# Optimization experiments

Hardware: AMD Instinct MI355X
Metric: run time of the kernel (lower is better)

Reference implementation:

```python
import jax, jax.numpy as jnp
import numpy as np

N, E, D, H, C = 20000, 320000, 128, 4, 128
NEG_SLOPE = 0.2

def _ln(x, g, b, eps=1e-5):
    mu = x.mean(-1, keepdims=True)
    var = ((x - mu) ** 2).mean(-1, keepdims=True)
    return (x - mu) * jax.lax.rsqrt(var + eps) * g + b

def _gatv2(x, src, dst, Wl, bl, Wr, br, att, b):
    # PyG GATv2Conv, concat=False (mean over heads), dropout off (eval)
    n = x.shape[0]
    xl = (x @ Wl + bl).reshape(n, H, C)   # source transform
    xr = (x @ Wr + br).reshape(n, H, C)   # destination transform
    e = jax.nn.leaky_relu(xl[src] + xr[dst], NEG_SLOPE)      # [E,H,C]
    score = jnp.einsum('ehc,hc->eh', e, att)                 # [E,H]
    m = jax.ops.segment_max(score, dst, num_segments=n)      # per-dst max
    w = jnp.exp(score - m[dst])
    denom = jax.ops.segment_sum(w, dst, num_segments=n)
    alpha = w / (denom[dst] + 1e-16)                         # softmax over incoming edges
    out = jax.ops.segment_sum(alpha[:, :, None] * xl[src], dst, num_segments=n)  # [N,H,C]
    return out.mean(axis=1) + b

def setup_inputs() -> dict:
    key = jax.random.key(0)
    ks = jax.random.split(key, 34)
    s = 1.0 / np.sqrt(D)
    def w(k, shape):
        return jax.random.normal(k, shape, jnp.float32) * s
    inp = {
        'x': jax.random.normal(ks[0], (N, D), jnp.float32),
        'edge_index': jax.random.randint(ks[1], (2, E), 0, N, jnp.int32),
        'W_in': w(ks[2], (D, C)), 'b_in': jnp.zeros((C,), jnp.float32),
        'c1_Wl': w(ks[3], (C, H * C)), 'c1_bl': jnp.zeros((H * C,), jnp.float32),
        'c1_Wr': w(ks[4], (C, H * C)), 'c1_br': jnp.zeros((H * C,), jnp.float32),
        'c1_att': w(ks[5], (H, C)), 'c1_b': jnp.zeros((C,), jnp.float32),
        'ln1_g': jnp.ones((C,), jnp.float32), 'ln1_b': jnp.zeros((C,), jnp.float32),
        'a_Wl': w(ks[6], (C, H * C)), 'a_bl': jnp.zeros((H * C,), jnp.float32),
        'a_Wr': w(ks[7], (C, H * C)), 'a_br': jnp.zeros((H * C,), jnp.float32),
        'a_att': w(ks[8], (H, C)), 'a_b': jnp.zeros((C,), jnp.float32),
        'aln_g': jnp.ones((C,), jnp.float32), 'aln_b': jnp.zeros((C,), jnp.float32),
        'ah_W': w(ks[9], (C, 1)), 'ah_b': jnp.zeros((1,), jnp.float32),
        'k_Wl': w(ks[10], (C, H * C)), 'k_bl': jnp.zeros((H * C,), jnp.float32),
        'k_Wr': w(ks[11], (C, H * C)), 'k_br': jnp.zeros((H * C,), jnp.float32),
        'k_att': w(ks[12], (H, C)), 'k_b': jnp.zeros((C,), jnp.float32),
        'kln_g': jnp.ones((C,), jnp.float32), 'kln_b': jnp.zeros((C,), jnp.float32),
        'kh_W': w(ks[13], (C, 1)), 'kh_b': jnp.zeros((1,), jnp.float32),
    }
    return inp

def reference(x, edge_index, W_in, b_in,
              c1_Wl, c1_bl, c1_Wr, c1_br, c1_att, c1_b, ln1_g, ln1_b,
              a_Wl, a_bl, a_Wr, a_br, a_att, a_b, aln_g, aln_b, ah_W, ah_b,
              k_Wl, k_bl, k_Wr, k_br, k_att, k_b, kln_g, kln_b, kh_W, kh_b):
    n = x.shape[0]
    loops = jnp.arange(n, dtype=edge_index.dtype)
    src = jnp.concatenate([edge_index[0], loops])  # PyG adds self-loops by default
    dst = jnp.concatenate([edge_index[1], loops])
    h = jax.nn.relu(x @ W_in + b_in)
    h_res = _gatv2(h, src, dst, c1_Wl, c1_bl, c1_Wr, c1_br, c1_att, c1_b)
    h = jax.nn.relu(_ln(h + h_res, ln1_g, ln1_b))
    xa = _gatv2(h, src, dst, a_Wl, a_bl, a_Wr, a_br, a_att, a_b)
    xa = jax.nn.relu(_ln(xa + h, aln_g, aln_b))
    action_logits = (xa @ ah_W + ah_b).squeeze(-1)
    xc = _gatv2(h, src, dst, k_Wl, k_bl, k_Wr, k_br, k_att, k_b)
    xc = jax.nn.relu(_ln(xc + h, kln_g, kln_b))
    state_value = xc @ kh_W + kh_b
    return action_logits, state_value
```

## Files before the change

### kernel.cpp

```cpp
#include <hip/hip_runtime.h>
#include <hip/hip_bf16.h>

typedef __hip_bfloat16 bf16;
typedef __attribute__((ext_vector_type(8))) short short8;
typedef __attribute__((ext_vector_type(4))) short short4_t;
typedef __attribute__((ext_vector_type(4))) float float4_t;
typedef __attribute__((ext_vector_type(2))) float float2v;
typedef __attribute__((ext_vector_type(2))) unsigned int uint2v;

__device__ __forceinline__ short f2bs(float f) {
    bf16 b = __float2bfloat16(f);
    return *(short*)&b;
}

template <int CTRL>
__device__ __forceinline__ float dpp_addf(float x) {
    int s = __builtin_amdgcn_update_dpp(
        0, __builtin_bit_cast(int, x), CTRL, 0xf, 0xf, true);
    return x + __builtin_bit_cast(float, s);
}
__device__ __forceinline__ float rowsum16(float x) {
    x = dpp_addf<0xB1>(x);
    x = dpp_addf<0x4E>(x);
    x = dpp_addf<0x141>(x);
    x = dpp_addf<0x140>(x);
    return x;
}

__global__ __launch_bounds__(256) void count_kernel(const int* __restrict__ ei,
                                                    int* __restrict__ cnt,
                                                    int E, int N, int NB) {
    int e = blockIdx.x * 256 + threadIdx.x;
    if (e >= E + N) return;
    int s, d;
    if (e < E) { s = ei[e]; d = ei[(size_t)E + e]; }
    else       { s = e - E; d = e - E; }
    atomicAdd(&cnt[(size_t)d * NB + (s >> 10)], 1);
}

__global__ __launch_bounds__(256) void scan_blk_kernel(const int* __restrict__ cnt,
                                                       int* __restrict__ rowptr,
                                                       int* __restrict__ bsum, int M) {
    __shared__ int ts[256];
    const int tid = threadIdx.x;
    const int idx = blockIdx.x * 1024 + tid * 4;
    int v[4];
    int s = 0;
#pragma unroll
    for (int i = 0; i < 4; ++i) {
        int j = idx + i;
        v[i] = (j < M) ? cnt[j] : 0;
        s += v[i];
    }
    ts[tid] = s;
    __syncthreads();
    for (int off = 1; off < 256; off <<= 1) {
        int t = (tid >= off) ? ts[tid - off] : 0;
        __syncthreads();
        ts[tid] += t;
        __syncthreads();
    }
    int run = (tid == 0) ? 0 : ts[tid - 1];
    if (tid == 255) bsum[blockIdx.x] = ts[255];
#pragma unroll
    for (int i = 0; i < 4; ++i) {
        int j = idx + i;
        if (j < M) rowptr[j] = run;
        run += v[i];
    }
}

__global__ __launch_bounds__(1024) void scan_top_kernel(int* __restrict__ bsum, int NBLK) {
    __shared__ int ps[1024];
    const int tid = threadIdx.x;
    int v = (tid < NBLK) ? bsum[tid] : 0;
    ps[tid] = v;
    __syncthreads();
    for (int off = 1; off < 1024; off <<= 1) {
        int t = (tid >= off) ? ps[tid - off] : 0;
        __syncthreads();
        ps[tid] += t;
        __syncthreads();
    }
    int ex = (tid == 0) ? 0 : ps[tid - 1];
    if (tid < NBLK) bsum[tid] = ex;
}

__global__ __launch_bounds__(256) void scan_add_kernel(int* __restrict__ rowptr,
                                                       const int* __restrict__ bsum,
                                                       int M, int ET) {
    int idx = blockIdx.x * 256 + threadIdx.x;
    if (idx < M) rowptr[idx] += bsum[idx >> 10];
    if (idx == 0) rowptr[M] = ET;
}

__global__ __launch_bounds__(256) void scatter_kernel(const int* __restrict__ ei,
                                                      const int* __restrict__ rowptr,
                                                      int* __restrict__ cursor,
                                                      int* __restrict__ csr_off,
                                                      int E, int N, int NB) {
    int e = blockIdx.x * 256 + threadIdx.x;
    if (e >= E + N) return;
    int s, d;
    if (e < E) { s = ei[e]; d = ei[(size_t)E + e]; }
    else       { s = e - E; d = e - E; }
    size_t b = (size_t)d * NB + (s >> 10);
    int pos = atomicAdd(&cursor[b], 1);
    csr_off[rowptr[b] + pos] = s * 4096;
}

__global__ __launch_bounds__(256) void transpose_w_kernel(
        const float* __restrict__ W_in,
        const float* __restrict__ c1_Wl, const float* __restrict__ c1_Wr,
        const float* __restrict__ a_Wl, const float* __restrict__ a_Wr,
        const float* __restrict__ k_Wl, const float* __restrict__ k_Wr,
        bf16* __restrict__ Wt,
        const float* __restrict__ c1_bl, const float* __restrict__ c1_br,
        const float* __restrict__ a_bl, const float* __restrict__ a_br,
        const float* __restrict__ k_bl, const float* __restrict__ k_br,
        float* __restrict__ b1, float* __restrict__ bak) {
    if (blockIdx.z == 7) {
        int flat = blockIdx.y * 16 + blockIdx.x;
        if (flat >= 12) return;
        int i = flat * 256 + threadIdx.x;
        if (i < 1024) {
            b1[i] = (i < 512) ? c1_bl[i] : c1_br[i - 512];
        } else if (i < 3072) {
            int j = i - 1024;
            const float* b = (j < 512) ? a_bl : (j < 1024) ? a_br
                           : (j < 1536) ? k_bl : k_br;
            bak[j] = b[j & 511];
        }
        return;
    }
    __shared__ float tile[32][33];
    const float* src; int nc, drow;
    switch (blockIdx.z) {
        case 0: src = W_in;  nc = 128; drow = 0;    break;
        case 1: src = c1_Wl; nc = 512; drow = 128;  break;
        case 2: src = c1_Wr; nc = 512; drow = 640;  break;
        case 3: src = a_Wl;  nc = 512; drow = 1152; break;
        case 4: src = a_Wr;  nc = 512; drow = 1664; break;
        case 5: src = k_Wl;  nc = 512; drow = 2176; break;
        default: src = k_Wr; nc = 512; drow = 2688; break;
    }
    const int n0 = blockIdx.x * 32;
    if (n0 >= nc) return;
    const int k0 = blockIdx.y * 32;
    const int tx = threadIdx.x & 31, ty = threadIdx.x >> 5;
#pragma unroll
    for (int i = 0; i < 4; ++i)
        tile[ty + i * 8][tx] = src[(size_t)(k0 + ty + i * 8) * nc + n0 + tx];
    __syncthreads();
#pragma unroll
    for (int i = 0; i < 4; ++i)
        Wt[(size_t)(drow + n0 + ty + i * 8) * 128 + k0 + tx] =
            __float2bfloat16(tile[tx][ty + i * 8]);
}

__global__ __launch_bounds__(256, 2) void gemm_mfma_kernel(
        const float* __restrict__ A, const bf16* __restrict__ Ab,
        const bf16* __restrict__ Wt,
        const float* __restrict__ bias,
        float* __restrict__ outF, bf16* __restrict__ outB,
        int M, int ldc, int relu) {
    __shared__ short As[128][136];
    __shared__ short Bs[128][136];
    const int tid = threadIdx.x;
    const int m0 = blockIdx.x * 128;
    const int n0 = blockIdx.y * 128;

    if (Ab) {
        short8 zero8;
#pragma unroll
        for (int q = 0; q < 8; ++q) zero8[q] = 0;
#pragma unroll
        for (int i = 0; i < 8; ++i) {
            int idx = i * 256 + tid;
            int r = idx >> 4, k8 = (idx & 15) * 8;
            int gm = m0 + r;
            short8 s = (gm < M) ? *(const short8*)&Ab[(size_t)gm * 128 + k8] : zero8;
            *(short8*)&As[r][k8] = s;
        }
    } else {
#pragma unroll
        for (int i = 0; i < 16; ++i) {
            int idx = i * 256 + tid;
            int r = idx >> 5, k4 = (idx & 31) * 4;
            int gm = m0 + r;
            float4 v = (gm < M) ? *(const float4*)&A[(size_t)gm * 128 + k4]
                                : make_float4(0.f, 0.f, 0.f, 0.f);
            short4_t s;
            s.x = f2bs(v.x); s.y = f2bs(v.y); s.z = f2bs(v.z); s.w = f2bs(v.w);
            *(short4_t*)&As[r][k4] = s;
        }
    }
#pragma unroll
    for (int i = 0; i < 8; ++i) {
        int idx = i * 256 + tid;
        int nr = idx >> 4, k8 = (idx & 15) * 8;
        *(short8*)&Bs[nr][k8] = *(const short8*)&Wt[(size_t)(n0 + nr) * 128 + k8];
    }
    __syncthreads();

    const int lane = tid & 63;
    const int w = tid >> 6;
    const int wm = (w >> 1) * 64, wn = (w & 1) * 64;
    const int fr = lane & 15;
    const int fq = (lane >> 4) * 8;

    float4_t acc[4][4] = {};
#pragma unroll
    for (int kk = 0; kk < 128; kk += 32) {
        short8 a[4], b[4];
#pragma unroll
        for (int t = 0; t < 4; ++t) a[t] = *(const short8*)&As[wm + t * 16 + fr][kk + fq];
#pragma unroll
        for (int t = 0; t < 4; ++t) b[t] = *(const short8*)&Bs[wn + t * 16 + fr][kk + fq];
#pragma unroll
        for (int ti = 0; ti < 4; ++ti)
#pragma unroll
            for (int tj = 0; tj < 4; ++tj)
                acc[ti][tj] = __builtin_amdgcn_mfma_f32_16x16x32_bf16(
                    a[ti], b[tj], acc[ti][tj], 0, 0, 0);
    }

    const int r0 = (lane >> 4) * 4;
#pragma unroll
    for (int ti = 0; ti < 4; ++ti) {
#pragma unroll
        for (int tj = 0; tj < 4; ++tj) {
            int col = n0 + wn + tj * 16 + fr;
            float bz = bias[col];
#pragma unroll
            for (int r = 0; r < 4; ++r) {
                size_t row = m0 + wm + ti * 16 + r0 + r;
                float v = acc[ti][tj][r] + bz;
                if (relu) v = fmaxf(v, 0.f);
                if (outF) outF[row * ldc + col] = v;
                if (outB) outB[row * ldc + col] = __float2bfloat16(v);
            }
        }
    }
}

__global__ __launch_bounds__(256) void gat_kernel(
        const bf16* __restrict__ xl, const bf16* __restrict__ xr,
        const float* __restrict__ att,
        const int* __restrict__ rowptr, const int* __restrict__ csr_off,
        const float* __restrict__ h_res,
        const float* __restrict__ gbias,
        const float* __restrict__ ln_g, const float* __restrict__ ln_b,
        float* __restrict__ h_out, bf16* __restrict__ h_outb, int N, int NB) {
    const int n = blockIdx.x * 4 + (threadIdx.x >> 6);
    if (n >= N) return;
    const int lane = threadIdx.x & 63;
    const int sl = lane & 15;
    const int hc = (lane >> 4) * 128 + sl * 8;

    float2v a2[4], xr2[4];
    {
        const float* ap = att + hc;
        short8 v = *(const short8*)(xr + (size_t)n * 2048 + hc);
        const unsigned int* uv = (const unsigned int*)&v;
#pragma unroll
        for (int j = 0; j < 4; ++j) {
            a2[j].x = ap[2 * j]; a2[j].y = ap[2 * j + 1];
            unsigned u = uv[j];
            xr2[j].x = __uint_as_float(u << 16);
            xr2[j].y = __uint_as_float(u & 0xffff0000u);
        }
    }
    const int rs = rowptr[(size_t)n * NB];
    const int re = rowptr[(size_t)n * NB + NB];
    const char* xlh = (const char*)xl + (size_t)hc * 2;

    float l = 0.f;
    float2v acc2[4] = {};
    int o0 = csr_off[rs];
    short8 va = *(const short8*)(xlh + o0);
    int o1 = (rs + 1 < re) ? csr_off[rs + 1] : o0;
    short8 vb = *(const short8*)(xlh + o1);
    int o2 = (rs + 2 < re) ? csr_off[rs + 2] : o0;

    for (int e = rs; e < re; ++e) {
        short8 cur = va; va = vb;
        if (e + 2 < re) {
            vb = *(const short8*)(xlh + o2);
            o2 = (e + 3 < re) ? csr_off[e + 3] : o0;
        }
        const unsigned int* uv = (const unsigned int*)&cur;
        float2v pa = {0.f, 0.f}, pb = {0.f, 0.f};
        float2v xs[4];
#pragma unroll
        for (int j = 0; j < 4; ++j) {
            unsigned u = uv[j];
            float2v x;
            x.x = __uint_as_float(u << 16);
            x.y = __uint_as_float(u & 0xffff0000u);
            xs[j] = x;
            float2v t = x + xr2[j];
            float2v ta = __builtin_bit_cast(float2v,
                           __builtin_bit_cast(uint2v, t) & 0x7fffffffu);
            pa = __builtin_elementwise_fma(a2[j], t, pa);
            pb = __builtin_elementwise_fma(a2[j], ta, pb);
        }
        float p = rowsum16(0.6f * (pa.x + pa.y) + 0.4f * (pb.x + pb.y));
        float wv = __expf(fminf(p, 60.f));
        l += wv;
        float2v ws = {wv, wv};
#pragma unroll
        for (int j = 0; j < 4; ++j)
            acc2[j] = __builtin_elementwise_fma(ws, xs[j], acc2[j]);
    }

    float* accf = (float*)acc2;
    const float inv = 0.25f / (l + 1e-16f);
#pragma unroll
    for (int j = 0; j < 8; ++j) accf[j] *= inv;
#pragma unroll
    for (int off = 16; off <= 32; off <<= 1)
#pragma unroll
        for (int j = 0; j < 8; ++j) accf[j] += __shfl_xor(accf[j], off, 64);

    if (lane < 16) {
        const int cb = sl * 8;
        const float* hr = h_res + (size_t)n * 128 + cb;
        float vv[8];
#pragma unroll
        for (int j = 0; j < 8; ++j) vv[j] = accf[j] + gbias[cb + j] + hr[j];
        float t1 = 0.f, t2 = 0.f;
#pragma unroll
        for (int j = 0; j < 8; ++j) { t1 += vv[j]; t2 += vv[j] * vv[j]; }
        const float s1 = rowsum16(t1), s2 = rowsum16(t2);
        const float mu   = s1 * 0.0078125f;
        const float var  = s2 * 0.0078125f - mu * mu;
        const float rstd = rsqrtf(var + 1e-5f);
        float y[8];
#pragma unroll
        for (int j = 0; j < 8; ++j) {
            y[j] = fmaf((vv[j] - mu) * rstd, ln_g[cb + j], ln_b[cb + j]);
            y[j] = fmaxf(y[j], 0.f);
        }
        *(float4*)(h_out + (size_t)n * 128 + cb) = make_float4(y[0], y[1], y[2], y[3]);
        *(float4*)(h_out + (size_t)n * 128 + cb + 4) = make_float4(y[4], y[5], y[6], y[7]);
        short8 yb;
#pragma unroll
        for (int j = 0; j < 8; ++j) yb[j] = f2bs(y[j]);
        *(short8*)(h_outb + (size_t)n * 128 + cb) = yb;
    }
}

__global__ __launch_bounds__(256) void gat2_kernel(
        const bf16* __restrict__ cat,
        const float* __restrict__ a_att, const float* __restrict__ k_att,
        const int* __restrict__ rowptr, const int* __restrict__ csr_off,
        const float* __restrict__ h_res,
        const float* __restrict__ a_gb, const float* __restrict__ k_gb,
        const float* __restrict__ aln_g, const float* __restrict__ aln_b,
        const float* __restrict__ kln_g, const float* __restrict__ kln_b,
        const float* __restrict__ ah_W, const float* __restrict__ ah_b,
        const float* __restrict__ kh_W, const float* __restrict__ kh_b,
        float* __restrict__ out_logits, float* __restrict__ out_value,
        int N, int NB) {
    const int n = blockIdx.x * 4 + (threadIdx.x >> 6);
    if (n >= N) return;
    const int lane = threadIdx.x & 63;
    const int sl = lane & 15;
    const int hc = (lane >> 4) * 128 + sl * 8;

    float2v aa[4], ak[4], xra[4], xrk[4];
    {
        const float* apa = a_att + hc;
        const float* apk = k_att + hc;
        short8 vra = *(const short8*)(cat + (size_t)n * 2048 + 512 + hc);
        short8 vrk = *(const short8*)(cat + (size_t)n * 2048 + 1536 + hc);
        const unsigned int* ua = (const unsigned int*)&vra;
        const unsigned int* uk = (const unsigned int*)&vrk;
#pragma unroll
        for (int j = 0; j < 4; ++j) {
            aa[j].x = apa[2 * j]; aa[j].y = apa[2 * j + 1];
            ak[j].x = apk[2 * j]; ak[j].y = apk[2 * j + 1];
            unsigned u = ua[j];
            xra[j].x = __uint_as_float(u << 16);
            xra[j].y = __uint_as_float(u & 0xffff0000u);
            u = uk[j];
            xrk[j].x = __uint_as_float(u << 16);
            xrk[j].y = __uint_as_float(u & 0xffff0000u);
        }
    }
    const int rs = rowptr[(size_t)n * NB];
    const int re = rowptr[(size_t)n * NB + NB];
    const char* xlh = (const char*)cat + (size_t)hc * 2;

    float la = 0.f, lk = 0.f;
    float2v acca[4] = {}, acck[4] = {};
    int o0 = csr_off[rs];
    short8 vaa = *(const short8*)(xlh + o0);
    short8 vak = *(const short8*)(xlh + o0 + 2048);
    int o1 = (rs + 1 < re) ? csr_off[rs + 1] : o0;
    short8 vba = *(const short8*)(xlh + o1);
    short8 vbk = *(const short8*)(xlh + o1 + 2048);
    int o2 = (rs + 2 < re) ? csr_off[rs + 2] : o0;

    for (int e = rs; e < re; ++e) {
        short8 ca = vaa, ck = vak;
        vaa = vba; vak = vbk;
        if (e + 2 < re) {
            vba = *(const short8*)(xlh + o2);
            vbk = *(const short8*)(xlh + o2 + 2048);
            o2 = (e + 3 < re) ? csr_off[e + 3] : o0;
        }
        const unsigned int* ua = (const unsigned int*)&ca;
        const unsigned int* uk = (const unsigned int*)&ck;
        float2v paa = {0.f, 0.f}, pba = {0.f, 0.f};
        float2v pak = {0.f, 0.f}, pbk = {0.f, 0.f};
        float2v xsa[4], xsk[4];
#pragma unroll
        for (int j = 0; j < 4; ++j) {
            unsigned u = ua[j];
            float2v x;
            x.x = __uint_as_float(u << 16);
            x.y = __uint_as_float(u & 0xffff0000u);
            xsa[j] = x;
            float2v t = x + xra[j];
            float2v ta = __builtin_bit_cast(float2v,
                           __builtin_bit_cast(uint2v, t) & 0x7fffffffu);
            paa = __builtin_elementwise_fma(aa[j], t, paa);
            pba = __builtin_elementwise_fma(aa[j], ta, pba);

            u = uk[j];
            x.x = __uint_as_float(u << 16);
            x.y = __uint_as_float(u & 0xffff0000u);
            xsk[j] = x;
            t = x + xrk[j];
            ta = __builtin_bit_cast(float2v,
                   __builtin_bit_cast(uint2v, t) & 0x7fffffffu);
            pak = __builtin_elementwise_fma(ak[j], t, pak);
            pbk = __builtin_elementwise_fma(ak[j], ta, pbk);
        }
        float p_a = rowsum16(0.6f * (paa.x + paa.y) + 0.4f * (pba.x + pba.y));
        float p_k = rowsum16(0.6f * (pak.x + pak.y) + 0.4f * (pbk.x + pbk.y));
        float wa = __expf(fminf(p_a, 60.f));
        float wk = __expf(fminf(p_k, 60.f));
        la += wa; lk += wk;
        float2v wsa = {wa, wa}, wsk = {wk, wk};
#pragma unroll
        for (int j = 0; j < 4; ++j) {
            acca[j] = __builtin_elementwise_fma(wsa, xsa[j], acca[j]);
            acck[j] = __builtin_elementwise_fma(wsk, xsk[j], acck[j]);
        }
    }

    float* afa = (float*)acca;
    float* afk = (float*)acck;
    const float inva = 0.25f / (la + 1e-16f);
    const float invk = 0.25f / (lk + 1e-16f);
#pragma unroll
    for (int j = 0; j < 8; ++j) { afa[j] *= inva; afk[j] *= invk; }
#pragma unroll
    for (int off = 16; off <= 32; off <<= 1)
#pragma unroll
        for (int j = 0; j < 8; ++j) {
            afa[j] += __shfl_xor(afa[j], off, 64);
            afk[j] += __shfl_xor(afk[j], off, 64);
        }

    if (lane < 32) {
        const int cb = sl * 8;
        const float* hr = h_res + (size_t)n * 128 + cb;
        float hrv[8];
#pragma unroll
        for (int j = 0; j < 8; ++j) hrv[j] = hr[j];
        if (lane < 16) {
            float vv[8];
#pragma unroll
            for (int j = 0; j < 8; ++j) vv[j] = afa[j] + a_gb[cb + j] + hrv[j];
            float t1 = 0.f, t2 = 0.f;
#pragma unroll
            for (int j = 0; j < 8; ++j) { t1 += vv[j]; t2 += vv[j] * vv[j]; }
            const float s1 = rowsum16(t1), s2 = rowsum16(t2);
            const float mu   = s1 * 0.0078125f;
            const float var  = s2 * 0.0078125f - mu * mu;
            const float rstd = rsqrtf(var + 1e-5f);
            float d = 0.f;
#pragma unroll
            for (int j = 0; j < 8; ++j) {
                float y = fmaf((vv[j] - mu) * rstd, aln_g[cb + j], aln_b[cb + j]);
                d += fmaxf(y, 0.f) * ah_W[cb + j];
            }
            d = rowsum16(d);
            if (sl == 0) out_logits[n] = d + ah_b[0];
        } else {
            float vv[8];
#pragma unroll
            for (int j = 0; j < 8; ++j) vv[j] = afk[j] + k_gb[cb + j] + hrv[j];
            float t1 = 0.f, t2 = 0.f;
#pragma unroll
            for (int j = 0; j < 8; ++j) { t1 += vv[j]; t2 += vv[j] * vv[j]; }
            const float s1 = rowsum16(t1), s2 = rowsum16(t2);
            const float mu   = s1 * 0.0078125f;
            const float var  = s2 * 0.0078125f - mu * mu;
            const float rstd = rsqrtf(var + 1e-5f);
            float d = 0.f;
#pragma unroll
            for (int j = 0; j < 8; ++j) {
                float y = fmaf((vv[j] - mu) * rstd, kln_g[cb + j], kln_b[cb + j]);
                d += fmaxf(y, 0.f) * kh_W[cb + j];
            }
            d = rowsum16(d);
            if (sl == 0) out_value[n] = d + kh_b[0];
        }
    }
}

extern "C" void kernel_launch(void* const* d_in, const int* in_sizes, int n_in,
                              void* d_out, int out_size, void* d_ws, size_t ws_size,
                              hipStream_t stream) {
    const float* x      = (const float*)d_in[0];
    const int*   ei     = (const int*)  d_in[1];
    const float* W_in   = (const float*)d_in[2];
    const float* b_in   = (const float*)d_in[3];
    const float* c1_Wl  = (const float*)d_in[4];
    const float* c1_bl  = (const float*)d_in[5];
    const float* c1_Wr  = (const float*)d_in[6];
    const float* c1_br  = (const float*)d_in[7];
    const float* c1_att = (const float*)d_in[8];
    const float* c1_b   = (const float*)d_in[9];
    const float* ln1_g  = (const float*)d_in[10];
    const float* ln1_b  = (const float*)d_in[11];
    const float* a_Wl   = (const float*)d_in[12];
    const float* a_bl   = (const float*)d_in[13];
    const float* a_Wr   = (const float*)d_in[14];
    const float* a_br   = (const float*)d_in[15];
    const float* a_att  = (const float*)d_in[16];
    const float* a_b    = (const float*)d_in[17];
    const float* aln_g  = (const float*)d_in[18];
    const float* aln_b  = (const float*)d_in[19];
    const float* ah_W   = (const float*)d_in[20];
    const float* ah_b   = (const float*)d_in[21];
    const float* k_Wl   = (const float*)d_in[22];
    const float* k_bl   = (const float*)d_in[23];
    const float* k_Wr   = (const float*)d_in[24];
    const float* k_br   = (const float*)d_in[25];
    const float* k_att  = (const float*)d_in[26];
    const float* k_b    = (const float*)d_in[27];
    const float* kln_g  = (const float*)d_in[28];
    const float* kln_b  = (const float*)d_in[29];
    const float* kh_W   = (const float*)d_in[30];
    const float* kh_b   = (const float*)d_in[31];

    const int N  = in_sizes[0] / 128;
    const int E  = in_sizes[1] / 2;
    const int ET = E + N;
    const int MB = (N + 127) / 128;
    const int Npad = MB * 128;
    const int NB = (N + 1023) >> 10;
    const int M  = N * NB;
    const int NBLK = (M + 1023) / 1024;

    char* ws = (char*)d_ws;
    size_t off = 0;
    auto alloc = [&](size_t bytes) -> void* {
        void* p = ws + off;
        off += (bytes + 255) & ~(size_t)255;
        return p;
    };
    int*   rowptr  = (int*)alloc((size_t)(M + 1) * 4);
    int*   cntcur  = (int*)alloc((size_t)2 * M * 4);
    int*   bsum    = (int*)alloc((size_t)NBLK * 4);
    int*   csr_off = (int*)alloc((size_t)ET * 4);
    float* h0      = (float*)alloc((size_t)Npad * 128 * 4);
    bf16*  h0b     = (bf16*)alloc((size_t)Npad * 128 * 2);
    float* h1      = (float*)alloc((size_t)Npad * 128 * 4);
    bf16*  h1b     = (bf16*)alloc((size_t)Npad * 128 * 2);
    bf16*  Wt      = (bf16*)alloc((size_t)3200 * 128 * 2);
    float* b1cat   = (float*)alloc(1024 * 4);
    float* bakcat  = (float*)alloc(2048 * 4);
    bf16*  cat     = (bf16*)alloc((size_t)Npad * 2048 * 2);

    int* cnt    = cntcur;
    int* cursor = cntcur + M;
    const bf16* Wt_in = Wt;
    const bf16* Wt_1  = Wt + 128 * 128;
    const bf16* Wt_ak = Wt + 128 * 128 + 1024 * 128;

    float* out_logits = (float*)d_out;
    float* out_value  = (float*)d_out + N;

    hipMemsetAsync(cntcur, 0, (size_t)2 * M * 4, stream);
    count_kernel<<<(ET + 255) / 256, 256, 0, stream>>>(ei, cnt, E, N, NB);
    transpose_w_kernel<<<dim3(16, 4, 8), 256, 0, stream>>>(
        W_in, c1_Wl, c1_Wr, a_Wl, a_Wr, k_Wl, k_Wr, Wt,
        c1_bl, c1_br, a_bl, a_br, k_bl, k_br, b1cat, bakcat);
    scan_blk_kernel<<<NBLK, 256, 0, stream>>>(cnt, rowptr, bsum, M);
    scan_top_kernel<<<1, 1024, 0, stream>>>(bsum, NBLK);
    scan_add_kernel<<<(M + 255) / 256, 256, 0, stream>>>(rowptr, bsum, M, ET);
    scatter_kernel<<<(ET + 255) / 256, 256, 0, stream>>>(ei, rowptr, cursor, csr_off,
                                                         E, N, NB);

    gemm_mfma_kernel<<<dim3(MB, 1), 256, 0, stream>>>(x, nullptr, Wt_in, b_in,
                                                      h0, h0b, N, 128, 1);
    gemm_mfma_kernel<<<dim3(MB, 8), 256, 0, stream>>>(nullptr, h0b, Wt_1, b1cat,
                                                      nullptr, cat, Npad, 2048, 0);
    gat_kernel<<<(N + 3) / 4, 256, 0, stream>>>(cat, cat + 512, c1_att, rowptr, csr_off,
                                      h0, c1_b, ln1_g, ln1_b, h1, h1b, N, NB);
    gemm_mfma_kernel<<<dim3(MB, 16), 256, 0, stream>>>(nullptr, h1b, Wt_ak, bakcat,
                                                       nullptr, cat, Npad, 2048, 0);
    gat2_kernel<<<(N + 3) / 4, 256, 0, stream>>>(cat, a_att, k_att, rowptr, csr_off,
                                      h1, a_b, k_b, aln_g, aln_b, kln_g, kln_b,
                                      ah_W, ah_b, kh_W, kh_b,
                                      out_logits, out_value, N, NB);
}
```

Baseline: 392.2 us.

## Use plain per-destination CSR and force packed FP32 FMA in GAT loops

Replaces the (destination, source-block) bucketed CSR with a plain per-destination CSR. This shrinks the count/cursor/rowptr arrays from N*NB entries to N and makes the memset, scan and scatter kernels much smaller. It drops the grouping of each node's edges by source block, which may have improved gather locality in the GAT kernels. The inner GAT loops now emit v_pk_fma_f32 and v_pk_add_f32 through inline asm so the compiler cannot split them into scalar ops.

```diff
diff --git a/kernel.cpp b/kernel.cpp
--- a/kernel.cpp
+++ b/kernel.cpp
@@ -13,6 +13,17 @@
     return *(short*)&b;
 }
 
+__device__ __forceinline__ float2v pk_fma(float2v a, float2v b, float2v c) {
+    float2v d;
+    asm("v_pk_fma_f32 %0, %1, %2, %3" : "=v"(d) : "v"(a), "v"(b), "v"(c));
+    return d;
+}
+__device__ __forceinline__ float2v pk_add(float2v a, float2v b) {
+    float2v d;
+    asm("v_pk_add_f32 %0, %1, %2" : "=v"(d) : "v"(a), "v"(b));
+    return d;
+}
+
 template <int CTRL>
 __device__ __forceinline__ float dpp_addf(float x) {
     int s = __builtin_amdgcn_update_dpp(
@@ -28,14 +39,11 @@
 }
 
 __global__ __launch_bounds__(256) void count_kernel(const int* __restrict__ ei,
-                                                    int* __restrict__ cnt,
-                                                    int E, int N, int NB) {
+                                                    int* __restrict__ cnt, int E, int N) {
     int e = blockIdx.x * 256 + threadIdx.x;
     if (e >= E + N) return;
-    int s, d;
-    if (e < E) { s = ei[e]; d = ei[(size_t)E + e]; }
-    else       { s = e - E; d = e - E; }
-    atomicAdd(&cnt[(size_t)d * NB + (s >> 10)], 1);
+    int d = (e < E) ? ei[(size_t)E + e] : (e - E);
+    atomicAdd(&cnt[d], 1);
 }
 
 __global__ __launch_bounds__(256) void scan_blk_kernel(const int* __restrict__ cnt,
@@ -98,15 +106,14 @@
                                                       const int* __restrict__ rowptr,
                                                       int* __restrict__ cursor,
                                                       int* __restrict__ csr_off,
-                                                      int E, int N, int NB) {
+                                                      int E, int N) {
     int e = blockIdx.x * 256 + threadIdx.x;
     if (e >= E + N) return;
     int s, d;
     if (e < E) { s = ei[e]; d = ei[(size_t)E + e]; }
     else       { s = e - E; d = e - E; }
-    size_t b = (size_t)d * NB + (s >> 10);
-    int pos = atomicAdd(&cursor[b], 1);
-    csr_off[rowptr[b] + pos] = s * 4096;
+    int pos = atomicAdd(&cursor[d], 1);
+    csr_off[rowptr[d] + pos] = s * 4096;
 }
 
 __global__ __launch_bounds__(256) void transpose_w_kernel(
@@ -251,7 +258,7 @@
         const float* __restrict__ h_res,
         const float* __restrict__ gbias,
         const float* __restrict__ ln_g, const float* __restrict__ ln_b,
-        float* __restrict__ h_out, bf16* __restrict__ h_outb, int N, int NB) {
+        float* __restrict__ h_out, bf16* __restrict__ h_outb, int N) {
     const int n = blockIdx.x * 4 + (threadIdx.x >> 6);
     if (n >= N) return;
     const int lane = threadIdx.x & 63;
@@ -271,8 +278,7 @@
             xr2[j].y = __uint_as_float(u & 0xffff0000u);
         }
     }
-    const int rs = rowptr[(size_t)n * NB];
-    const int re = rowptr[(size_t)n * NB + NB];
+    const int rs = rowptr[n], re = rowptr[n + 1];
     const char* xlh = (const char*)xl + (size_t)hc * 2;
 
     float l = 0.f;
@@ -299,11 +305,11 @@
             x.x = __uint_as_float(u << 16);
             x.y = __uint_as_float(u & 0xffff0000u);
             xs[j] = x;
-            float2v t = x + xr2[j];
+            float2v t = pk_add(x, xr2[j]);
             float2v ta = __builtin_bit_cast(float2v,
                            __builtin_bit_cast(uint2v, t) & 0x7fffffffu);
-            pa = __builtin_elementwise_fma(a2[j], t, pa);
-            pb = __builtin_elementwise_fma(a2[j], ta, pb);
+            pa = pk_fma(a2[j], t, pa);
+            pb = pk_fma(a2[j], ta, pb);
         }
         float p = rowsum16(0.6f * (pa.x + pa.y) + 0.4f * (pb.x + pb.y));
         float wv = __expf(fminf(p, 60.f));
@@ -311,7 +317,7 @@
         float2v ws = {wv, wv};
 #pragma unroll
         for (int j = 0; j < 4; ++j)
-            acc2[j] = __builtin_elementwise_fma(ws, xs[j], acc2[j]);
+            acc2[j] = pk_fma(ws, xs[j], acc2[j]);
     }
 
     float* accf = (float*)acc2;
@@ -361,8 +367,7 @@
         const float* __restrict__ kln_g, const float* __restrict__ kln_b,
         const float* __restrict__ ah_W, const float* __restrict__ ah_b,
         const float* __restrict__ kh_W, const float* __restrict__ kh_b,
-        float* __restrict__ out_logits, float* __restrict__ out_value,
-        int N, int NB) {
+        float* __restrict__ out_logits, float* __restrict__ out_value, int N) {
     const int n = blockIdx.x * 4 + (threadIdx.x >> 6);
     if (n >= N) return;
     const int lane = threadIdx.x & 63;
@@ -389,8 +394,7 @@
             xrk[j].y = __uint_as_float(u & 0xffff0000u);
         }
     }
-    const int rs = rowptr[(size_t)n * NB];
-    const int re = rowptr[(size_t)n * NB + NB];
+    const int rs = rowptr[n], re = rowptr[n + 1];
     const char* xlh = (const char*)cat + (size_t)hc * 2;
 
     float la = 0.f, lk = 0.f;
@@ -423,21 +427,21 @@
             x.x = __uint_as_float(u << 16);
             x.y = __uint_as_float(u & 0xffff0000u);
             xsa[j] = x;
-            float2v t = x + xra[j];
+            float2v t = pk_add(x, xra[j]);
             float2v ta = __builtin_bit_cast(float2v,
                            __builtin_bit_cast(uint2v, t) & 0x7fffffffu);
-            paa = __builtin_elementwise_fma(aa[j], t, paa);
-            pba = __builtin_elementwise_fma(aa[j], ta, pba);
+            paa = pk_fma(aa[j], t, paa);
+            pba = pk_fma(aa[j], ta, pba);
 
             u = uk[j];
             x.x = __uint_as_float(u << 16);
             x.y = __uint_as_float(u & 0xffff0000u);
             xsk[j] = x;
-            t = x + xrk[j];
+            t = pk_add(x, xrk[j]);
             ta = __builtin_bit_cast(float2v,
                    __builtin_bit_cast(uint2v, t) & 0x7fffffffu);
-            pak = __builtin_elementwise_fma(ak[j], t, pak);
-            pbk = __builtin_elementwise_fma(ak[j], ta, pbk);
+            pak = pk_fma(ak[j], t, pak);
+            pbk = pk_fma(ak[j], ta, pbk);
         }
         float p_a = rowsum16(0.6f * (paa.x + paa.y) + 0.4f * (pba.x + pba.y));
         float p_k = rowsum16(0.6f * (pak.x + pak.y) + 0.4f * (pbk.x + pbk.y));
@@ -447,8 +451,8 @@
         float2v wsa = {wa, wa}, wsk = {wk, wk};
 #pragma unroll
         for (int j = 0; j < 4; ++j) {
-            acca[j] = __builtin_elementwise_fma(wsa, xsa[j], acca[j]);
-            acck[j] = __builtin_elementwise_fma(wsk, xsk[j], acck[j]);
+            acca[j] = pk_fma(wsa, xsa[j], acca[j]);
+            acck[j] = pk_fma(wsk, xsk[j], acck[j]);
         }
     }
 
@@ -555,9 +559,7 @@
     const int ET = E + N;
     const int MB = (N + 127) / 128;
     const int Npad = MB * 128;
-    const int NB = (N + 1023) >> 10;
-    const int M  = N * NB;
-    const int NBLK = (M + 1023) / 1024;
+    const int NBLK = (N + 1023) / 1024;
 
     char* ws = (char*)d_ws;
     size_t off = 0;
@@ -566,8 +568,8 @@
         off += (bytes + 255) & ~(size_t)255;
         return p;
     };
-    int*   rowptr  = (int*)alloc((size_t)(M + 1) * 4);
-    int*   cntcur  = (int*)alloc((size_t)2 * M * 4);
+    int*   rowptr  = (int*)alloc((size_t)(N + 1) * 4);
+    int*   cntcur  = (int*)alloc((size_t)2 * N * 4);
     int*   bsum    = (int*)alloc((size_t)NBLK * 4);
     int*   csr_off = (int*)alloc((size_t)ET * 4);
     float* h0      = (float*)alloc((size_t)Npad * 128 * 4);
@@ -580,7 +582,7 @@
     bf16*  cat     = (bf16*)alloc((size_t)Npad * 2048 * 2);
 
     int* cnt    = cntcur;
-    int* cursor = cntcur + M;
+    int* cursor = cntcur + N;
     const bf16* Wt_in = Wt;
     const bf16* Wt_1  = Wt + 128 * 128;
     const bf16* Wt_ak = Wt + 128 * 128 + 1024 * 128;
@@ -588,27 +590,26 @@
     float* out_logits = (float*)d_out;
     float* out_value  = (float*)d_out + N;
 
-    hipMemsetAsync(cntcur, 0, (size_t)2 * M * 4, stream);
-    count_kernel<<<(ET + 255) / 256, 256, 0, stream>>>(ei, cnt, E, N, NB);
+    hipMemsetAsync(cntcur, 0, (size_t)2 * N * 4, stream);
+    count_kernel<<<(ET + 255) / 256, 256, 0, stream>>>(ei, cnt, E, N);
     transpose_w_kernel<<<dim3(16, 4, 8), 256, 0, stream>>>(
         W_in, c1_Wl, c1_Wr, a_Wl, a_Wr, k_Wl, k_Wr, Wt,
         c1_bl, c1_br, a_bl, a_br, k_bl, k_br, b1cat, bakcat);
-    scan_blk_kernel<<<NBLK, 256, 0, stream>>>(cnt, rowptr, bsum, M);
+    scan_blk_kernel<<<NBLK, 256, 0, stream>>>(cnt, rowptr, bsum, N);
     scan_top_kernel<<<1, 1024, 0, stream>>>(bsum, NBLK);
-    scan_add_kernel<<<(M + 255) / 256, 256, 0, stream>>>(rowptr, bsum, M, ET);
-    scatter_kernel<<<(ET + 255) / 256, 256, 0, stream>>>(ei, rowptr, cursor, csr_off,
-                                                         E, N, NB);
+    scan_add_kernel<<<(N + 255) / 256, 256, 0, stream>>>(rowptr, bsum, N, ET);
+    scatter_kernel<<<(ET + 255) / 256, 256, 0, stream>>>(ei, rowptr, cursor, csr_off, E, N);
 
     gemm_mfma_kernel<<<dim3(MB, 1), 256, 0, stream>>>(x, nullptr, Wt_in, b_in,
                                                       h0, h0b, N, 128, 1);
     gemm_mfma_kernel<<<dim3(MB, 8), 256, 0, stream>>>(nullptr, h0b, Wt_1, b1cat,
                                                       nullptr, cat, Npad, 2048, 0);
     gat_kernel<<<(N + 3) / 4, 256, 0, stream>>>(cat, cat + 512, c1_att, rowptr, csr_off,
-                                      h0, c1_b, ln1_g, ln1_b, h1, h1b, N, NB);
+                                      h0, c1_b, ln1_g, ln1_b, h1, h1b, N);
     gemm_mfma_kernel<<<dim3(MB, 16), 256, 0, stream>>>(nullptr, h1b, Wt_ak, bakcat,
                                                        nullptr, cat, Npad, 2048, 0);
     gat2_kernel<<<(N + 3) / 4, 256, 0, stream>>>(cat, a_att, k_att, rowptr, csr_off,
                                       h1, a_b, k_b, aln_g, aln_b, kln_g, kln_b,
                                       ah_W, ah_b, kh_W, kh_b,
-                                      out_logits, out_value, N, NB);
-}
+                                      out_logits, out_value, N);
+}
```

Result: no change. 395.7 us (+0.9%).
